# Performance work log

Measured on AMD Instinct MI355X. Metric: run time of the kernel, lower is better.

The kernel has to match this reference:

```python
import jax, jax.numpy as jnp
import numpy as np

TAU = 1.0            # temperature (self.temperature.item())
FAST_WEIGHT_DECAY = 0.01
FAST_WEIGHT_LR = 0.01

B, IN, H = 128, 1024, 1024


def setup_inputs() -> dict:
    key = jax.random.key(0)
    k = jax.random.split(key, 6)
    scale_ih = 1.0 / np.sqrt(IN)
    scale_hh = np.sqrt(2.0 / (H + H))  # xavier_uniform-like std
    return {
        "x_t": jax.random.normal(k[0], (B, IN), jnp.float32),
        "h_prev": jax.random.normal(k[1], (B, H), jnp.float32),
        "W_ih": jax.random.normal(k[2], (H, IN), jnp.float32) * scale_ih,
        "b_ih": jnp.zeros((H,), jnp.float32),
        "W_hh_fixed": jax.random.normal(k[3], (H, H), jnp.float32) * scale_hh,
        "W_hh_virtual": jnp.zeros((H, H), jnp.float32),
        "gumbel_u": jax.random.uniform(k[4], (B, H, H), jnp.float32),
    }


def reference(x_t, h_prev, W_ih, b_ih, W_hh_fixed, W_hh_virtual, gumbel_u):
    # input contribution: Linear(input_size, hidden_size)
    input_contrib = x_t @ W_ih.T + b_ih                      # (B, H)

    # logits scaled by temperature once, then gumbel_softmax divides by tau again
    logits = (W_hh_fixed + W_hh_virtual) / TAU               # (H, H)
    eps = 1e-9
    g = -jnp.log(-jnp.log(jnp.clip(gumbel_u, eps, 1.0 - eps)))  # Gumbel(0,1), (B,H,H)
    y = jax.nn.softmax((logits[None, :, :] + g) / TAU, axis=2)  # soft sampling, (B,H,H)

    # weighted exchange: each output neuron o reduces sampled weights against h_prev
    contrib = jnp.einsum('boh,bh->bo', y, h_prev)            # (B, H)
    h_next = jnp.tanh(input_contrib + contrib)               # (B, H)

    # Hebbian fast-weight update (no_grad in original)
    hebbian = jnp.einsum('bo,bh->oh', h_next, h_prev) / B    # mean over batch, (H,H)
    W_hh_virtual_new = jax.lax.stop_gradient(
        W_hh_virtual * (1.0 - FAST_WEIGHT_DECAY) + hebbian * FAST_WEIGHT_LR
    )
    return h_next, W_hh_virtual_new
```

## Files before the change

kernel.cpp:

```cpp
#include <hip/hip_runtime.h>
#include <hip/hip_bf16.h>
#include <cstddef>

#define B_DIM  128
#define IN_DIM 1024
#define H_DIM  1024

constexpr float kInvTau  = 1.0f;
constexpr float kDecay   = 1.0f - 0.01f;
constexpr float kLrOverB = 0.01f / 128.0f;

__global__ __launch_bounds__(256) void fused_rows(
    const float* __restrict__ x_t,
    const float* __restrict__ h_prev,
    const float* __restrict__ W_ih,
    const float* __restrict__ b_ih,
    const float* __restrict__ W_f,
    const float* __restrict__ W_v,
    const float* __restrict__ gu,
    float* __restrict__ h_next)
{
    const int o  = blockIdx.x;
    const int bc = blockIdx.y;
    const int t  = threadIdx.x;

    __shared__ __align__(16) float lrow[H_DIM];
    __shared__ __align__(16) float wrow[H_DIM];

    {
        const float4 a = reinterpret_cast<const float4*>(W_f + (size_t)o * H_DIM)[t];
        const float4 b = reinterpret_cast<const float4*>(W_v + (size_t)o * H_DIM)[t];
        float4 s;
        s.x = a.x + b.x; s.y = a.y + b.y; s.z = a.z + b.z; s.w = a.w + b.w;
        reinterpret_cast<float4*>(lrow)[t] = s;
        reinterpret_cast<float4*>(wrow)[t] =
            reinterpret_cast<const float4*>(W_ih + (size_t)o * IN_DIM)[t];
    }
    __syncthreads();

    const float bias = b_ih[o];
    const int w = t >> 6, lane = t & 63;

    const float4* l4 = reinterpret_cast<const float4*>(lrow);
    const float4* w4 = reinterpret_cast<const float4*>(wrow);

    for (int bi = 0; bi < 8; ++bi) {
        const int b = bc * 32 + bi * 4 + w;

        const float4* g4  = reinterpret_cast<const float4*>(gu + ((size_t)b * H_DIM + o) * H_DIM);
        const float4* hp4 = reinterpret_cast<const float4*>(h_prev + (size_t)b * H_DIM);
        const float4* x4  = reinterpret_cast<const float4*>(x_t + (size_t)b * IN_DIM);

        float s[16], hp[16];
        float m  = -3.0e38f;
        float ic = 0.0f;

#pragma unroll
        for (int j = 0; j < 4; ++j) {
            const int idx = lane + 64 * j;
            const float4 u  = g4[idx];
            const float4 l  = l4[idx];
            const float4 p  = hp4[idx];
            const float4 xv = x4[idx];
            const float4 wv = w4[idx];

            const float ub[4] = {u.x, u.y, u.z, u.w};
            const float lb[4] = {l.x, l.y, l.z, l.w};
            const float pb[4] = {p.x, p.y, p.z, p.w};
            const float xb[4] = {xv.x, xv.y, xv.z, xv.w};
            const float wb[4] = {wv.x, wv.y, wv.z, wv.w};

#pragma unroll
            for (int c = 0; c < 4; ++c) {
                const float uc  = fmaxf(ub[c], 1e-9f);
                const float gmb = -__logf(-__logf(uc));
                const float sv  = (lb[c] * kInvTau + gmb) * kInvTau;
                s[4 * j + c]  = sv;
                hp[4 * j + c] = pb[c];
                m  = fmaxf(m, sv);
                ic = fmaf(xb[c], wb[c], ic);
            }
        }

#pragma unroll
        for (int off = 32; off > 0; off >>= 1) {
            m  = fmaxf(m, __shfl_xor(m, off, 64));
            ic += __shfl_xor(ic, off, 64);
        }

        float sum = 0.0f, dot = 0.0f;
#pragma unroll
        for (int i = 0; i < 16; ++i) {
            const float e = __expf(s[i] - m);
            sum += e;
            dot = fmaf(e, hp[i], dot);
        }
#pragma unroll
        for (int off = 32; off > 0; off >>= 1) {
            sum += __shfl_xor(sum, off, 64);
            dot += __shfl_xor(dot, off, 64);
        }

        if (lane == 0) {
            h_next[(size_t)b * H_DIM + o] = tanhf(ic + bias + dot / sum);
        }
    }
}

__global__ __launch_bounds__(256) void hebbian_update(
    const float* __restrict__ h_next,
    const float* __restrict__ h_prev,
    const float* __restrict__ W_v,
    float* __restrict__ W_out)
{
    const int h0 = blockIdx.x * 64;
    const int o0 = blockIdx.y * 64;
    const int t  = threadIdx.x;

    __shared__ __align__(16) float hn_s[B_DIM][64];
    __shared__ __align__(16) float hp_s[B_DIM][64];

#pragma unroll
    for (int i = 0; i < 32; ++i) {
        const int e  = t + 256 * i;
        const int bb = e >> 6;
        const int cc = e & 63;
        hn_s[bb][cc] = h_next[(size_t)bb * H_DIM + o0 + cc];
        hp_s[bb][cc] = h_prev[(size_t)bb * H_DIM + h0 + cc];
    }
    __syncthreads();

    const int tx = t & 15;
    const int ty = t >> 4;

    float acc[4][4] = {{0.f}};

#pragma unroll 8
    for (int b = 0; b < B_DIM; ++b) {
        const float4 av = reinterpret_cast<const float4*>(hn_s[b])[ty];
        const float4 bv = reinterpret_cast<const float4*>(hp_s[b])[tx];
        const float aa[4] = {av.x, av.y, av.z, av.w};
        const float bb[4] = {bv.x, bv.y, bv.z, bv.w};
#pragma unroll
        for (int a = 0; a < 4; ++a)
#pragma unroll
            for (int c = 0; c < 4; ++c)
                acc[a][c] = fmaf(aa[a], bb[c], acc[a][c]);
    }

#pragma unroll
    for (int a = 0; a < 4; ++a) {
        const int o = o0 + 4 * ty + a;
        const size_t base = (size_t)o * H_DIM + h0 + 4 * tx;
        const float4 wv = *reinterpret_cast<const float4*>(W_v + base);
        float4 r;
        r.x = wv.x * kDecay + acc[a][0] * kLrOverB;
        r.y = wv.y * kDecay + acc[a][1] * kLrOverB;
        r.z = wv.z * kDecay + acc[a][2] * kLrOverB;
        r.w = wv.w * kDecay + acc[a][3] * kLrOverB;
        *reinterpret_cast<float4*>(W_out + base) = r;
    }
}

extern "C" void kernel_launch(void* const* d_in, const int* in_sizes, int n_in,
                              void* d_out, int out_size, void* d_ws, size_t ws_size,
                              hipStream_t stream)
{
    const float* x_t    = (const float*)d_in[0];
    const float* h_prev = (const float*)d_in[1];
    const float* W_ih   = (const float*)d_in[2];
    const float* b_ih   = (const float*)d_in[3];
    const float* W_f    = (const float*)d_in[4];
    const float* W_v    = (const float*)d_in[5];
    const float* gu     = (const float*)d_in[6];

    float* out    = (float*)d_out;
    float* h_next = out;
    float* W_out  = out + (size_t)B_DIM * H_DIM;

    fused_rows<<<dim3(H_DIM, B_DIM / 32), 256, 0, stream>>>(
        x_t, h_prev, W_ih, b_ih, W_f, W_v, gu, h_next);

    hebbian_update<<<dim3(H_DIM / 64, H_DIM / 64), 256, 0, stream>>>(
        h_next, h_prev, W_v, W_out);
}
```

Baseline: 166.4 us.

## Rewrite Gumbel softmax as exp(logit)/(-log u) and split input GEMM out

Uses the identity exp(l - log(-log u)) = exp(l)/(-log u), which removes one log per element, the max pass and the second exp pass. The exp of the logits is precomputed once per block for 8 output rows and reused across the batch tile. The input projection x_t @ W_ih^T moves into a separate tiled GEMM kernel that writes to workspace, instead of being recomputed redundantly inside every row block. Dropping the max subtraction risks overflow if logits are large, and the change adds an extra kernel launch and a workspace round trip.

```diff
diff --git a/kernel.cpp b/kernel.cpp
--- a/kernel.cpp
+++ b/kernel.cpp
@@ -6,95 +6,139 @@
 #define IN_DIM 1024
 #define H_DIM  1024
 
-constexpr float kInvTau  = 1.0f;
 constexpr float kDecay   = 1.0f - 0.01f;
 constexpr float kLrOverB = 0.01f / 128.0f;
 
-__global__ __launch_bounds__(256) void fused_rows(
+__global__ __launch_bounds__(256) void input_gemm(
     const float* __restrict__ x_t,
-    const float* __restrict__ h_prev,
     const float* __restrict__ W_ih,
     const float* __restrict__ b_ih,
+    float* __restrict__ ic)
+{
+    const int o0 = blockIdx.x * 64;
+    const int b0 = blockIdx.y * 16;
+    const int t  = threadIdx.x;
+
+    __shared__ float Wt[64][68];
+    __shared__ float xs[64][17];
+
+    const int tx = t & 15;
+    const int ty = t >> 4;
+
+    float acc[4] = {0.f, 0.f, 0.f, 0.f};
+
+    for (int kc = 0; kc < IN_DIM / 64; ++kc) {
+        const int k0 = kc * 64;
+
+#pragma unroll
+        for (int ii = 0; ii < 4; ++ii) {
+            const int i  = t + 256 * ii;
+            const int r  = i >> 4;
+            const int c4 = (i & 15) * 4;
+            const float4 wv = *reinterpret_cast<const float4*>(
+                &W_ih[(size_t)(o0 + r) * IN_DIM + k0 + c4]);
+            Wt[c4 + 0][r] = wv.x; Wt[c4 + 1][r] = wv.y;
+            Wt[c4 + 2][r] = wv.z; Wt[c4 + 3][r] = wv.w;
+        }
+        {
+            const int br = t >> 4;
+            const int c4 = (t & 15) * 4;
+            const float4 xv = *reinterpret_cast<const float4*>(
+                &x_t[(size_t)(b0 + br) * IN_DIM + k0 + c4]);
+            xs[c4 + 0][br] = xv.x; xs[c4 + 1][br] = xv.y;
+            xs[c4 + 2][br] = xv.z; xs[c4 + 3][br] = xv.w;
+        }
+        __syncthreads();
+
+#pragma unroll 8
+        for (int k = 0; k < 64; ++k) {
+            const float  xb = xs[k][ty];
+            const float4 wv = *reinterpret_cast<const float4*>(&Wt[k][4 * tx]);
+            acc[0] = fmaf(wv.x, xb, acc[0]);
+            acc[1] = fmaf(wv.y, xb, acc[1]);
+            acc[2] = fmaf(wv.z, xb, acc[2]);
+            acc[3] = fmaf(wv.w, xb, acc[3]);
+        }
+        __syncthreads();
+    }
+
+    const int o = o0 + 4 * tx;
+    const int b = b0 + ty;
+    float4 r;
+    r.x = acc[0] + b_ih[o + 0];
+    r.y = acc[1] + b_ih[o + 1];
+    r.z = acc[2] + b_ih[o + 2];
+    r.w = acc[3] + b_ih[o + 3];
+    *reinterpret_cast<float4*>(&ic[(size_t)b * H_DIM + o]) = r;
+}
+
+__global__ __launch_bounds__(512, 4) void fused_rows(
+    const float* __restrict__ h_prev,
     const float* __restrict__ W_f,
     const float* __restrict__ W_v,
     const float* __restrict__ gu,
+    const float* __restrict__ ic,
     float* __restrict__ h_next)
 {
-    const int o  = blockIdx.x;
-    const int bc = blockIdx.y;
+    const int o0 = blockIdx.x * 8;
+    const int b0 = blockIdx.y * 8;
     const int t  = threadIdx.x;
 
-    __shared__ __align__(16) float lrow[H_DIM];
-    __shared__ __align__(16) float wrow[H_DIM];
-
-    {
-        const float4 a = reinterpret_cast<const float4*>(W_f + (size_t)o * H_DIM)[t];
-        const float4 b = reinterpret_cast<const float4*>(W_v + (size_t)o * H_DIM)[t];
-        float4 s;
-        s.x = a.x + b.x; s.y = a.y + b.y; s.z = a.z + b.z; s.w = a.w + b.w;
-        reinterpret_cast<float4*>(lrow)[t] = s;
-        reinterpret_cast<float4*>(wrow)[t] =
-            reinterpret_cast<const float4*>(W_ih + (size_t)o * IN_DIM)[t];
+    __shared__ __align__(16) float el[8 * H_DIM];
+
+#pragma unroll
+    for (int ii = 0; ii < 4; ++ii) {
+        const int i = t + 512 * ii;
+        const int r = i >> 8;
+        const int c = i & 255;
+        const size_t off = (size_t)(o0 + r) * H_DIM + 4 * c;
+        const float4 a = *reinterpret_cast<const float4*>(W_f + off);
+        const float4 b = *reinterpret_cast<const float4*>(W_v + off);
+        float4 e;
+        e.x = __expf(a.x + b.x); e.y = __expf(a.y + b.y);
+        e.z = __expf(a.z + b.z); e.w = __expf(a.w + b.w);
+        reinterpret_cast<float4*>(el)[i] = e;
     }
     __syncthreads();
 
-    const float bias = b_ih[o];
     const int w = t >> 6, lane = t & 63;
-
-    const float4* l4 = reinterpret_cast<const float4*>(lrow);
-    const float4* w4 = reinterpret_cast<const float4*>(wrow);
-
-    for (int bi = 0; bi < 8; ++bi) {
-        const int b = bc * 32 + bi * 4 + w;
-
-        const float4* g4  = reinterpret_cast<const float4*>(gu + ((size_t)b * H_DIM + o) * H_DIM);
-        const float4* hp4 = reinterpret_cast<const float4*>(h_prev + (size_t)b * H_DIM);
-        const float4* x4  = reinterpret_cast<const float4*>(x_t + (size_t)b * IN_DIM);
-
-        float s[16], hp[16];
-        float m  = -3.0e38f;
-        float ic = 0.0f;
-
+    const int b = b0 + w;
+
+    const float4* hp4 = reinterpret_cast<const float4*>(h_prev + (size_t)b * H_DIM);
+    float4 hp[4];
+#pragma unroll
+    for (int j = 0; j < 4; ++j) hp[j] = hp4[lane + 64 * j];
+
+    const float4* el4 = reinterpret_cast<const float4*>(el);
+
+#pragma unroll 2
+    for (int oi = 0; oi < 8; ++oi) {
+        const int o = o0 + oi;
+        const float4* g4 =
+            reinterpret_cast<const float4*>(gu + ((size_t)b * H_DIM + o) * H_DIM);
+
+        float sum = 0.f, dot = 0.f;
 #pragma unroll
         for (int j = 0; j < 4; ++j) {
-            const int idx = lane + 64 * j;
-            const float4 u  = g4[idx];
-            const float4 l  = l4[idx];
-            const float4 p  = hp4[idx];
-            const float4 xv = x4[idx];
-            const float4 wv = w4[idx];
-
-            const float ub[4] = {u.x, u.y, u.z, u.w};
-            const float lb[4] = {l.x, l.y, l.z, l.w};
-            const float pb[4] = {p.x, p.y, p.z, p.w};
-            const float xb[4] = {xv.x, xv.y, xv.z, xv.w};
-            const float wb[4] = {wv.x, wv.y, wv.z, wv.w};
-
-#pragma unroll
-            for (int c = 0; c < 4; ++c) {
-                const float uc  = fmaxf(ub[c], 1e-9f);
-                const float gmb = -__logf(-__logf(uc));
-                const float sv  = (lb[c] * kInvTau + gmb) * kInvTau;
-                s[4 * j + c]  = sv;
-                hp[4 * j + c] = pb[c];
-                m  = fmaxf(m, sv);
-                ic = fmaf(xb[c], wb[c], ic);
-            }
-        }
-
-#pragma unroll
-        for (int off = 32; off > 0; off >>= 1) {
-            m  = fmaxf(m, __shfl_xor(m, off, 64));
-            ic += __shfl_xor(ic, off, 64);
-        }
-
-        float sum = 0.0f, dot = 0.0f;
-#pragma unroll
-        for (int i = 0; i < 16; ++i) {
-            const float e = __expf(s[i] - m);
-            sum += e;
-            dot = fmaf(e, hp[i], dot);
-        }
+            const float4 u = g4[lane + 64 * j];
+            const float4 e = el4[oi * 256 + lane + 64 * j];
+            const float4 p = hp[j];
+
+            const float t0 = -__logf(fmaxf(u.x, 1e-9f));
+            const float t1 = -__logf(fmaxf(u.y, 1e-9f));
+            const float t2 = -__logf(fmaxf(u.z, 1e-9f));
+            const float t3 = -__logf(fmaxf(u.w, 1e-9f));
+            const float q0 = __fdividef(e.x, t0);
+            const float q1 = __fdividef(e.y, t1);
+            const float q2 = __fdividef(e.z, t2);
+            const float q3 = __fdividef(e.w, t3);
+            sum += q0 + q1 + q2 + q3;
+            dot = fmaf(q0, p.x, dot);
+            dot = fmaf(q1, p.y, dot);
+            dot = fmaf(q2, p.z, dot);
+            dot = fmaf(q3, p.w, dot);
+        }
+
 #pragma unroll
         for (int off = 32; off > 0; off >>= 1) {
             sum += __shfl_xor(sum, off, 64);
@@ -102,7 +146,8 @@
         }
 
         if (lane == 0) {
-            h_next[(size_t)b * H_DIM + o] = tanhf(ic + bias + dot / sum);
+            h_next[(size_t)b * H_DIM + o] =
+                tanhf(ic[(size_t)b * H_DIM + o] + dot / sum);
         }
     }
 }
@@ -177,9 +222,13 @@
     float* out    = (float*)d_out;
     float* h_next = out;
     float* W_out  = out + (size_t)B_DIM * H_DIM;
-
-    fused_rows<<<dim3(H_DIM, B_DIM / 32), 256, 0, stream>>>(
-        x_t, h_prev, W_ih, b_ih, W_f, W_v, gu, h_next);
+    float* ic     = (float*)d_ws;
+
+    input_gemm<<<dim3(H_DIM / 64, B_DIM / 16), 256, 0, stream>>>(
+        x_t, W_ih, b_ih, ic);
+
+    fused_rows<<<dim3(H_DIM / 8, B_DIM / 8), 512, 0, stream>>>(
+        h_prev, W_f, W_v, gu, ic, h_next);
 
     hebbian_update<<<dim3(H_DIM / 64, H_DIM / 64), 256, 0, stream>>>(
         h_next, h_prev, W_v, W_out);
```

Result: no change. 168.0 us (+1.0%).
